# Kernel optimization log

Measured on AMD Instinct MI355X. Metric: run time of the kernel, lower is better.

Reference implementation:

```python
import jax, jax.numpy as jnp
import numpy as np

H1, H2, H3 = 32, 64, 64
NODEN = 12
NODES_PER_GRAPH = NODEN + 2  # 14
N = 700000                   # 50000 graphs * 14 nodes
E = 4000000


def setup_inputs() -> dict:
    key = jax.random.key(0)
    ks = jax.random.split(key, 8)
    x = jax.random.normal(ks[0], (N, H1), dtype=jnp.float32)
    edges = jax.random.randint(ks[1], (2, E), 0, N, dtype=jnp.int64)
    W1 = jax.random.normal(ks[2], (H1, H2), dtype=jnp.float32) / np.sqrt(H1).astype(np.float32)
    b1 = jnp.zeros((H2,), jnp.float32)
    W2 = jax.random.normal(ks[3], (H2, H3), dtype=jnp.float32) / np.sqrt(H2).astype(np.float32)
    b2 = jnp.zeros((H3,), jnp.float32)
    Wfc = jax.random.normal(ks[4], (H3 * NODES_PER_GRAPH, 1), dtype=jnp.float32) / np.sqrt(H3 * NODES_PER_GRAPH).astype(np.float32)
    bfc = jnp.zeros((1,), jnp.float32)
    return {"x": x, "edges": edges, "W1": W1, "b1": b1, "W2": W2, "b2": b2, "Wfc": Wfc, "bfc": bfc}


def gcn_conv(x, src, dst, W, b, n):
    # PyG GCNConv: h = X W; add self-loops; norm = deg^-1/2[src]*deg^-1/2[dst]
    h = x @ W  # [N, out]
    ones = jnp.ones(src.shape[0], dtype=h.dtype)
    deg = jax.ops.segment_sum(ones, dst, num_segments=n) + jnp.asarray(1.0, h.dtype)  # +1 self-loop
    dinv = jax.lax.rsqrt(deg)  # deg >= 1 always (self-loop)
    norm = dinv[src] * dinv[dst]  # [E]
    agg = jax.ops.segment_sum(h[src] * norm[:, None], dst, num_segments=n)
    agg = agg + h * (dinv * dinv)[:, None]  # self-loop contribution
    return agg + b


def reference(x, edges, W1, b1, W2, b2, Wfc, bfc):
    src, dst = edges[0], edges[1]
    h = jax.nn.relu(gcn_conv(x, src, dst, W1, b1, N))
    # F.dropout(training=False) is identity in eval mode
    h = jax.nn.relu(gcn_conv(h, src, dst, W2, b2, N))
    h = h.reshape(-1, H3 * NODES_PER_GRAPH)  # [B, 896]
    return h @ Wfc + bfc  # [B, 1]
```

## Files before the change

### kernel.cpp

```cpp
#include <hip/hip_runtime.h>
#include <hip/hip_fp16.h>


typedef _Float16 half8 __attribute__((ext_vector_type(8)));
typedef float float4v __attribute__((ext_vector_type(4)));

#define CHUNK 8192
#define BSH 11
#define BNODES 2048

__global__ __launch_bounds__(256) void fallback_kernel(float* __restrict__ out, int n, float v)
{
  int i = blockIdx.x * 256 + threadIdx.x;
  if (i < n) out[i] = v;
}

__global__ __launch_bounds__(64) void probe_kernel(const int* __restrict__ edges, int* __restrict__ flag)
{
  if (threadIdx.x == 0) {
    int orv = edges[1] | edges[3] | edges[5] | edges[7] | edges[9] | edges[11] | edges[13] | edges[15];
    flag[0] = (orv == 0) ? 1 : 0;
  }
}

__global__ __launch_bounds__(64) void zero_dummy_kernel(
    __half* __restrict__ F1, __half* __restrict__ F2, int N)
{
  int t = threadIdx.x;
  if (t < 16) ((uint2*)(F1 + (size_t)N * 64))[t] = make_uint2(0, 0);
  else if (t < 32) ((uint2*)(F2 + (size_t)N * 64))[t - 16] = make_uint2(0, 0);
}

__global__ __launch_bounds__(256) void hist2_kernel(
    const int* __restrict__ edges, int E, int N, const int* __restrict__ flag,
    int* __restrict__ cnt, int NBK)
{
  __shared__ int lh[512];
  int t = threadIdx.x;
  int blk = blockIdx.x;
  for (int b = t; b < NBK; b += 256) lh[b] = 0;
  __syncthreads();
  int sh = flag[0];
  int base = blk * CHUNK;
#pragma unroll
  for (int k = 0; k < CHUNK / 256; k++) {
    int e = base + k * 256 + t;
    if (e < E) {
      int d = edges[(E + e) << sh];
      if ((unsigned)d < (unsigned)N) atomicAdd(&lh[d >> BSH], 1);
    }
  }
  __syncthreads();
  for (int b = t; b < NBK; b += 256) cnt[(size_t)blk * NBK + b] = lh[b];
}

__global__ __launch_bounds__(64) void colscan_kernel(
    int* __restrict__ cnt, int NCH, int NBK, int* __restrict__ totals)
{
  int b = blockIdx.x;
  int lane = threadIdx.x;
  int carry = 0;
  int rounds = (NCH + 63) >> 6;
  for (int r = 0; r < rounds; r++) {
    int blk = r * 64 + lane;
    int v = (blk < NCH) ? cnt[(size_t)blk * NBK + b] : 0;
    int incl = v;
#pragma unroll
    for (int off = 1; off < 64; off <<= 1) {
      int x = __shfl_up(incl, off);
      if (lane >= off) incl += x;
    }
    int excl = incl - v + carry;
    if (blk < NCH) cnt[(size_t)blk * NBK + b] = excl;
    carry += __shfl(incl, 63);
  }
  if (lane == 0) totals[b] = carry;
}

__global__ __launch_bounds__(512) void scan_totals_kernel(
    const int* __restrict__ totals, int NBK,
    int* __restrict__ bstart, int* __restrict__ rowptr, int N)
{
  __shared__ int sm[512];
  int t = threadIdx.x;
  int v = (t < NBK) ? totals[t] : 0;
  sm[t] = v;
  __syncthreads();
  for (int off = 1; off < 512; off <<= 1) {
    int x = 0;
    if (t >= off) x = sm[t - off];
    __syncthreads();
    if (t >= off) sm[t] += x;
    __syncthreads();
  }
  if (t < NBK) bstart[t] = sm[t] - v;
  if (t == 0) { bstart[NBK] = sm[511]; rowptr[N] = sm[511] + N; }
}

__global__ __launch_bounds__(256) void pass3_kernel(
    const int* __restrict__ edges, int E, int N, const int* __restrict__ flag,
    const int* __restrict__ cnt, const int* __restrict__ bstart,
    int* __restrict__ pair, int NBK)
{
  __shared__ int lcur[512];
  int t = threadIdx.x;
  int blk = blockIdx.x;
  for (int b = t; b < NBK; b += 256)
    lcur[b] = bstart[b] + cnt[(size_t)blk * NBK + b];
  __syncthreads();
  int sh = flag[0];
  int base = blk * CHUNK;
#pragma unroll
  for (int k = 0; k < CHUNK / 256; k++) {
    int e = base + k * 256 + t;
    if (e < E) {
      int s = edges[e << sh];
      int d = edges[(E + e) << sh];
      if ((unsigned)s < (unsigned)N && (unsigned)d < (unsigned)N) {
        int pos = atomicAdd(&lcur[d >> BSH], 1);
        pair[pos] = s | ((d & (BNODES - 1)) << 20);
      }
    }
  }
}

__global__ __launch_bounds__(256) void build_kernel(
    const int* __restrict__ pair, const int* __restrict__ bstart,
    int* __restrict__ rowptr, float* __restrict__ dinv, int* __restrict__ col, int N)
{
  __shared__ int hist[BNODES];
  __shared__ int cur[BNODES];
  __shared__ int sc[256];
  int b = blockIdx.x;
  int t = threadIdx.x;
  int pbeg = bstart[b], pend = bstart[b + 1];
  int colbase = pbeg + (b << BSH);
#pragma unroll
  for (int i = 0; i < BNODES / 256; i++) {
    int idx = i * 256 + t;
    int row = (b << BSH) + idx;
    hist[idx] = (row < N) ? 1 : 0;
  }
  __syncthreads();
  for (int p = pbeg + t; p < pend; p += 256)
    atomicAdd(&hist[(pair[p] >> 20) & (BNODES - 1)], 1);
  __syncthreads();
  int hv[8];
  int tsum = 0;
#pragma unroll
  for (int i = 0; i < 8; i++) { hv[i] = hist[t * 8 + i]; tsum += hv[i]; }
  sc[t] = tsum;
  __syncthreads();
  for (int off = 1; off < 256; off <<= 1) {
    int x = 0;
    if (t >= off) x = sc[t - off];
    __syncthreads();
    if (t >= off) sc[t] += x;
    __syncthreads();
  }
  int run = sc[t] - tsum;
#pragma unroll
  for (int i = 0; i < 8; i++) {
    int idx = t * 8 + i;
    int rp = colbase + run;
    int row = (b << BSH) + idx;
    if (row < N) {
      rowptr[row] = rp;
      dinv[row] = rsqrtf((float)hv[i]);
      col[rp] = row;
      cur[idx] = rp + 1;
    } else {
      cur[idx] = rp;
    }
    run += hv[i];
  }
  __syncthreads();
  for (int p = pbeg + t; p < pend; p += 256) {
    int v = pair[p];
    int pos = atomicAdd(&cur[(v >> 20) & (BNODES - 1)], 1);
    col[pos] = v & 0xFFFFF;
  }
}

__global__ __launch_bounds__(256) void mfma_mm1_kernel(
    const float* __restrict__ X, const float* __restrict__ W1,
    const float* __restrict__ dinv, __half* __restrict__ G, int n, int ntiles)
{
  int lane = threadIdx.x & 63;
  int n16 = lane & 15;
  int quad = lane >> 4;

  half8 bf[4];
#pragma unroll
  for (int jb = 0; jb < 4; jb++)
#pragma unroll
    for (int i = 0; i < 8; i++)
      bf[jb][i] = (_Float16)W1[(quad * 8 + i) * 64 + jb * 16 + n16];

  _Float16* Gh = (_Float16*)G;
  int wave = (blockIdx.x * 256 + threadIdx.x) >> 6;
  int nw = (gridDim.x * 256) >> 6;
  for (int tile = wave; tile < ntiles; tile += nw) {
    int ut = __builtin_amdgcn_readfirstlane(tile);
    int base = ut * 16;
    int node = base + n16;
    if (node >= n) node = n - 1;
    const float* xr = X + (size_t)node * 32 + quad * 8;
    half8 a;
#pragma unroll
    for (int i = 0; i < 8; i++) a[i] = (_Float16)xr[i];

    float4v acc[4];
#pragma unroll
    for (int jb = 0; jb < 4; jb++) {
      float4v z = {0.f, 0.f, 0.f, 0.f};
      acc[jb] = __builtin_amdgcn_mfma_f32_16x16x32_f16(a, bf[jb], z, 0, 0, 0);
    }
#pragma unroll
    for (int r = 0; r < 4; r++) {
      int node2 = base + quad * 4 + r;
      if (node2 < n) {
        float dv = dinv[node2];
#pragma unroll
        for (int jb = 0; jb < 4; jb++)
          Gh[(size_t)node2 * 64 + jb * 16 + n16] = (_Float16)(dv * acc[jb][r]);
      }
    }
  }
}

__device__ inline void hacc(uint4 v, __half2* a)
{
  a[0] = __hadd2(a[0], *reinterpret_cast<__half2*>(&v.x));
  a[1] = __hadd2(a[1], *reinterpret_cast<__half2*>(&v.y));
  a[2] = __hadd2(a[2], *reinterpret_cast<__half2*>(&v.z));
  a[3] = __hadd2(a[3], *reinterpret_cast<__half2*>(&v.w));
}

__device__ inline __half2 hrelu2(__half2 v)
{
  __half z = __float2half_rn(0.f);
  __half2 r;
  r.x = __hmax(v.x, z);
  r.y = __hmax(v.y, z);
  return r;
}

__global__ __launch_bounds__(256) void agg1_frag_kernel(
    const __half* __restrict__ G, const int* __restrict__ rowptr,
    const int* __restrict__ col, const float* __restrict__ dinv,
    const float* __restrict__ bias, __half* __restrict__ U, int ntiles, int ndummy)
{
  int lane = threadIdx.x & 63;
  int n16 = lane & 15;
  int quad = lane >> 4;

  const float* bp0 = bias + quad * 8;
  const float* bp1 = bias + 32 + quad * 8;
  float4 b0a = *(const float4*)bp0, b0b = *(const float4*)(bp0 + 4);
  float4 b1a = *(const float4*)bp1, b1b = *(const float4*)(bp1 + 4);
  __half2 bh0[4] = {__floats2half2_rn(b0a.x, b0a.y), __floats2half2_rn(b0a.z, b0a.w),
                    __floats2half2_rn(b0b.x, b0b.y), __floats2half2_rn(b0b.z, b0b.w)};
  __half2 bh1[4] = {__floats2half2_rn(b1a.x, b1a.y), __floats2half2_rn(b1a.z, b1a.w),
                    __floats2half2_rn(b1b.x, b1b.y), __floats2half2_rn(b1b.z, b1b.w)};

  const uint4* G4 = (const uint4*)G;
  uint4* U4 = (uint4*)U;
  int wave = (blockIdx.x * 256 + threadIdx.x) >> 6;
  int nw = (gridDim.x * 256) >> 6;
  for (int tile = wave; tile < ntiles; tile += nw) {
    int ut = __builtin_amdgcn_readfirstlane(tile);
    int node = ut * 16 + n16;
    int rbeg = rowptr[node];
    int rlen = rowptr[node + 1] - rbeg;

    __half2 z2 = __float2half2_rn(0.f);
    __half2 acc0[4] = {z2, z2, z2, z2};
    __half2 acc1[4] = {z2, z2, z2, z2};

    for (int j = 0; __any(j < rlen); j += 2) {
      int c0 = col[rbeg + j];
      int c1 = col[rbeg + j + 1];
      c0 = (j < rlen) ? c0 : ndummy;
      c1 = (j + 1 < rlen) ? c1 : ndummy;
      uint4 v00 = G4[((size_t)c0 << 3) + quad];
      uint4 v01 = G4[((size_t)c0 << 3) + 4 + quad];
      uint4 v10 = G4[((size_t)c1 << 3) + quad];
      uint4 v11 = G4[((size_t)c1 << 3) + 4 + quad];
      hacc(v00, acc0); hacc(v01, acc1);
      hacc(v10, acc0); hacc(v11, acc1);
    }

    __half2 dv = __half2half2(__float2half_rn(dinv[node]));
    uint4 o0, o1;
    __half2 r;
#pragma unroll
    for (int j = 0; j < 4; j++) {
      r = __hmul2(hrelu2(__hadd2(__hmul2(acc0[j], dv), bh0[j])), dv);
      (&o0.x)[j] = *reinterpret_cast<uint*>(&r);
      r = __hmul2(hrelu2(__hadd2(__hmul2(acc1[j], dv), bh1[j])), dv);
      (&o1.x)[j] = *reinterpret_cast<uint*>(&r);
    }
    U4[((size_t)node << 3) + quad] = o0;
    U4[((size_t)node << 3) + 4 + quad] = o1;
  }
}

__global__ __launch_bounds__(256) void out_init_kernel(
    float* __restrict__ out, const float* __restrict__ bfc, int n)
{
  int i = blockIdx.x * 256 + threadIdx.x;
  if (i < n) out[i] = bfc[0];
}

__global__ __launch_bounds__(256) void mfma_final_fused_kernel(
    const __half* __restrict__ U, const int* __restrict__ rowptr,
    const int* __restrict__ col, const float* __restrict__ dinv,
    const float* __restrict__ W2, const float* __restrict__ b2,
    const float* __restrict__ Wfc, float* __restrict__ out,
    int ntiles, int ndummy)
{
  int lane = threadIdx.x & 63;
  int n16 = lane & 15;
  int quad = lane >> 4;

  half8 bf[4][2];
#pragma unroll
  for (int jb = 0; jb < 4; jb++)
#pragma unroll
    for (int kf = 0; kf < 2; kf++)
#pragma unroll
      for (int i = 0; i < 8; i++)
        bf[jb][kf][i] = (_Float16)W2[(kf * 32 + quad * 8 + i) * 64 + jb * 16 + n16];
  float b2j[4];
#pragma unroll
  for (int jb = 0; jb < 4; jb++) b2j[jb] = b2[jb * 16 + n16];

  const uint4* U4 = (const uint4*)U;
  int wave = (blockIdx.x * 256 + threadIdx.x) >> 6;
  int nw = (gridDim.x * 256) >> 6;
  for (int tile = wave; tile < ntiles; tile += nw) {
    int ut = __builtin_amdgcn_readfirstlane(tile);
    int base = ut * 16;
    int node = base + n16;
    int rbeg = rowptr[node];
    int rlen = rowptr[node + 1] - rbeg;

    __half2 z2 = __float2half2_rn(0.f);
    __half2 acc0[4] = {z2, z2, z2, z2};
    __half2 acc1[4] = {z2, z2, z2, z2};

    for (int j = 0; __any(j < rlen); j += 2) {
      int c0 = col[rbeg + j];
      int c1 = col[rbeg + j + 1];
      c0 = (j < rlen) ? c0 : ndummy;
      c1 = (j + 1 < rlen) ? c1 : ndummy;
      uint4 v00 = U4[((size_t)c0 << 3) + quad];
      uint4 v01 = U4[((size_t)c0 << 3) + 4 + quad];
      uint4 v10 = U4[((size_t)c1 << 3) + quad];
      uint4 v11 = U4[((size_t)c1 << 3) + 4 + quad];
      hacc(v00, acc0); hacc(v01, acc1);
      hacc(v10, acc0); hacc(v11, acc1);
    }
    __half2 dv = __half2half2(__float2half_rn(dinv[node]));
#pragma unroll
    for (int j = 0; j < 4; j++) {
      acc0[j] = __hmul2(acc0[j], dv);
      acc1[j] = __hmul2(acc1[j], dv);
    }
    half8 a0 = *reinterpret_cast<half8*>(acc0);
    half8 a1 = *reinterpret_cast<half8*>(acc1);

    int g_r[4], t_r[4];
#pragma unroll
    for (int r = 0; r < 4; r++) {
      int nd = base + quad * 4 + r;
      g_r[r] = nd / 14;
      t_r[r] = nd - g_r[r] * 14;
    }
    float pr[4] = {0.f, 0.f, 0.f, 0.f};
#pragma unroll
    for (int jb = 0; jb < 4; jb++) {
      float4v acc = {0.f, 0.f, 0.f, 0.f};
      acc = __builtin_amdgcn_mfma_f32_16x16x32_f16(a0, bf[jb][0], acc, 0, 0, 0);
      acc = __builtin_amdgcn_mfma_f32_16x16x32_f16(a1, bf[jb][1], acc, 0, 0, 0);
      int j = jb * 16 + n16;
#pragma unroll
      for (int r = 0; r < 4; r++) {
        float h = acc[r] + b2j[jb];
        h = h > 0.f ? h : 0.f;
        pr[r] += h * Wfc[t_r[r] * 64 + j];
      }
    }
#pragma unroll
    for (int r = 0; r < 4; r++) {
#pragma unroll
      for (int off = 1; off < 16; off <<= 1) pr[r] += __shfl_xor(pr[r], off);
    }
    if (n16 == 0) {
#pragma unroll
      for (int r = 0; r < 4; r++) atomicAdd(&out[g_r[r]], pr[r]);
    }
  }
}

extern "C" void kernel_launch(void* const* d_in, const int* in_sizes, int n_in,
                              void* d_out, int out_size, void* d_ws, size_t ws_size,
                              hipStream_t stream)
{
  const float* x = (const float*)d_in[0];
  const int* edges = (const int*)d_in[1];
  const float* W1 = (const float*)d_in[2];
  const float* b1 = (const float*)d_in[3];
  const float* W2 = (const float*)d_in[4];
  const float* b2 = (const float*)d_in[5];
  const float* Wfc = (const float*)d_in[6];
  const float* bfc = (const float*)d_in[7];
  float* out = (float*)d_out;
  (void)n_in;

  const int N = in_sizes[0] / 32;
  const int E = in_sizes[1] / 2;
  const int B = out_size;
  const int NBK = (N + BNODES - 1) >> BSH;
  const int NCH = (E + CHUNK - 1) / CHUNK;

  char* ws = (char*)d_ws;
  size_t off = 0;
  auto alloc = [&](size_t bytes) -> void* {
    void* p = ws + off;
    off += (bytes + 255) & ~(size_t)255;
    return p;
  };
  int* flag = (int*)alloc(256);
  int* cnt = (int*)alloc((size_t)NCH * NBK * 4);
  int* totals = (int*)alloc((size_t)NBK * 4);
  int* bstart = (int*)alloc(((size_t)NBK + 1) * 4);
  int* col = (int*)alloc(((size_t)E + N + 256) * 4);
  int* rowptr = (int*)alloc(((size_t)N + 1) * 4);
  float* dinv = (float*)alloc((size_t)N * 4);
  __half* F1 = (__half*)alloc(((size_t)N + 16) * 64 * 2);
  __half* F2 = (__half*)alloc(((size_t)N + 16) * 64 * 2);
  int* pair = (int*)F1;

  if (off > ws_size) {
    float v = -(float)(double)(ws_size >> 20);
    fallback_kernel<<<(B + 255) / 256, 256, 0, stream>>>(out, B, v);
    return;
  }

  probe_kernel<<<1, 64, 0, stream>>>(edges, flag);
  zero_dummy_kernel<<<1, 64, 0, stream>>>(F1, F2, N);
  hist2_kernel<<<NCH, 256, 0, stream>>>(edges, E, N, flag, cnt, NBK);
  colscan_kernel<<<NBK, 64, 0, stream>>>(cnt, NCH, NBK, totals);
  scan_totals_kernel<<<1, 512, 0, stream>>>(totals, NBK, bstart, rowptr, N);
  pass3_kernel<<<NCH, 256, 0, stream>>>(edges, E, N, flag, cnt, bstart, pair, NBK);
  build_kernel<<<NBK, 256, 0, stream>>>(pair, bstart, rowptr, dinv, col, N);

  int ntiles = (N + 15) / 16;
  mfma_mm1_kernel<<<4096, 256, 0, stream>>>(x, W1, dinv, F1, N, ntiles);
  agg1_frag_kernel<<<4096, 256, 0, stream>>>(F1, rowptr, col, dinv, b1, F2, ntiles, N);
  out_init_kernel<<<(B + 255) / 256, 256, 0, stream>>>(out, bfc, B);
  mfma_final_fused_kernel<<<4096, 256, 0, stream>>>(F2, rowptr, col, dinv, W2, b2, Wfc,
                                                    out, ntiles, N);
}
```

Measured before the change: 573.1 us.

## Aggregate layer-1 on 32-wide scaled inputs before the W1 GEMM

Reorders layer 1 as (A·X)·W1 instead of A·(X·W1). A new kernel first scales X by dinv and stores it in fp16, so the gather loop reads 32 halves per neighbour instead of 64. The MFMA with W1, bias, ReLU and second scaling are then fused into the aggregation kernel. The neighbour loops in both aggregation kernels are also unrolled deeper (8 and 4 neighbours per step) with split accumulators to add memory-level parallelism. The trade-offs are extra padded dummy loads when node degrees are uneven and a different fp16 rounding order.

```diff
diff --git a/kernel.cpp b/kernel.cpp
--- a/kernel.cpp
+++ b/kernel.cpp
@@ -24,11 +24,11 @@
 }
 
 __global__ __launch_bounds__(64) void zero_dummy_kernel(
-    __half* __restrict__ F1, __half* __restrict__ F2, int N)
+    __half* __restrict__ P, __half* __restrict__ F2, int N)
 {
   int t = threadIdx.x;
-  if (t < 16) ((uint2*)(F1 + (size_t)N * 64))[t] = make_uint2(0, 0);
-  else if (t < 32) ((uint2*)(F2 + (size_t)N * 64))[t - 16] = make_uint2(0, 0);
+  if (t < 8) ((uint2*)(P + (size_t)N * 32))[t] = make_uint2(0, 0);
+  else if (t < 24) ((uint2*)(F2 + (size_t)N * 64))[t - 8] = make_uint2(0, 0);
 }
 
 __global__ __launch_bounds__(256) void hist2_kernel(
@@ -182,9 +182,40 @@
   }
 }
 
-__global__ __launch_bounds__(256) void mfma_mm1_kernel(
-    const float* __restrict__ X, const float* __restrict__ W1,
-    const float* __restrict__ dinv, __half* __restrict__ G, int n, int ntiles)
+__global__ __launch_bounds__(256) void scale_x_kernel(
+    const float* __restrict__ X, const float* __restrict__ dinv,
+    __half* __restrict__ P, int N)
+{
+  int idx = blockIdx.x * 256 + threadIdx.x;
+  int total = N * 4;
+  int stride = gridDim.x * 256;
+  for (int i = idx; i < total; i += stride) {
+    int node = i >> 2, part = i & 3;
+    const float4* xp = (const float4*)(X + (size_t)node * 32 + part * 8);
+    float dv = dinv[node];
+    float4 v0 = xp[0], v1 = xp[1];
+    half8 h;
+    h[0] = (_Float16)(dv * v0.x); h[1] = (_Float16)(dv * v0.y);
+    h[2] = (_Float16)(dv * v0.z); h[3] = (_Float16)(dv * v0.w);
+    h[4] = (_Float16)(dv * v1.x); h[5] = (_Float16)(dv * v1.y);
+    h[6] = (_Float16)(dv * v1.z); h[7] = (_Float16)(dv * v1.w);
+    *(half8*)(P + (size_t)node * 32 + part * 8) = h;
+  }
+}
+
+__device__ inline void hacc(uint4 v, __half2* a)
+{
+  a[0] = __hadd2(a[0], *reinterpret_cast<__half2*>(&v.x));
+  a[1] = __hadd2(a[1], *reinterpret_cast<__half2*>(&v.y));
+  a[2] = __hadd2(a[2], *reinterpret_cast<__half2*>(&v.z));
+  a[3] = __hadd2(a[3], *reinterpret_cast<__half2*>(&v.w));
+}
+
+__global__ __launch_bounds__(256) void agg1_mfma_kernel(
+    const __half* __restrict__ P, const int* __restrict__ rowptr,
+    const int* __restrict__ col, const float* __restrict__ dinv,
+    const float* __restrict__ W1, const float* __restrict__ b1,
+    __half* __restrict__ U, int ntiles, int ndummy)
 {
   int lane = threadIdx.x & 63;
   int n16 = lane & 15;
@@ -196,113 +227,59 @@
 #pragma unroll
     for (int i = 0; i < 8; i++)
       bf[jb][i] = (_Float16)W1[(quad * 8 + i) * 64 + jb * 16 + n16];
-
-  _Float16* Gh = (_Float16*)G;
+  float b1j[4];
+#pragma unroll
+  for (int jb = 0; jb < 4; jb++) b1j[jb] = b1[jb * 16 + n16];
+
+  const uint4* P4 = (const uint4*)P;
+  _Float16* Uh = (_Float16*)U;
   int wave = (blockIdx.x * 256 + threadIdx.x) >> 6;
   int nw = (gridDim.x * 256) >> 6;
   for (int tile = wave; tile < ntiles; tile += nw) {
     int ut = __builtin_amdgcn_readfirstlane(tile);
     int base = ut * 16;
     int node = base + n16;
-    if (node >= n) node = n - 1;
-    const float* xr = X + (size_t)node * 32 + quad * 8;
-    half8 a;
-#pragma unroll
-    for (int i = 0; i < 8; i++) a[i] = (_Float16)xr[i];
-
-    float4v acc[4];
+    int rbeg = rowptr[node];
+    int rlen = rowptr[node + 1] - rbeg;
+
+    __half2 z2 = __float2half2_rn(0.f);
+    __half2 aA[4] = {z2, z2, z2, z2};
+    __half2 aB[4] = {z2, z2, z2, z2};
+
+    for (int j = 0; __any(j < rlen); j += 8) {
+      int c[8];
+#pragma unroll
+      for (int q = 0; q < 8; q++) {
+        int cc = col[rbeg + j + q];
+        c[q] = (j + q < rlen) ? cc : ndummy;
+      }
+      uint4 v[8];
+#pragma unroll
+      for (int q = 0; q < 8; q++) v[q] = P4[((size_t)c[q] << 2) + quad];
+#pragma unroll
+      for (int q = 0; q < 8; q += 2) { hacc(v[q], aA); hacc(v[q + 1], aB); }
+    }
+#pragma unroll
+    for (int k = 0; k < 4; k++) aA[k] = __hadd2(aA[k], aB[k]);
+
+    half8 a = *reinterpret_cast<half8*>(aA);
+    float4v co[4];
 #pragma unroll
     for (int jb = 0; jb < 4; jb++) {
       float4v z = {0.f, 0.f, 0.f, 0.f};
-      acc[jb] = __builtin_amdgcn_mfma_f32_16x16x32_f16(a, bf[jb], z, 0, 0, 0);
+      co[jb] = __builtin_amdgcn_mfma_f32_16x16x32_f16(a, bf[jb], z, 0, 0, 0);
     }
 #pragma unroll
     for (int r = 0; r < 4; r++) {
       int node2 = base + quad * 4 + r;
-      if (node2 < n) {
-        float dv = dinv[node2];
-#pragma unroll
-        for (int jb = 0; jb < 4; jb++)
-          Gh[(size_t)node2 * 64 + jb * 16 + n16] = (_Float16)(dv * acc[jb][r]);
+      float dv = dinv[node2];
+#pragma unroll
+      for (int jb = 0; jb < 4; jb++) {
+        float h = dv * co[jb][r] + b1j[jb];
+        h = h > 0.f ? h : 0.f;
+        Uh[(size_t)node2 * 64 + jb * 16 + n16] = (_Float16)(dv * h);
       }
     }
-  }
-}
-
-__device__ inline void hacc(uint4 v, __half2* a)
-{
-  a[0] = __hadd2(a[0], *reinterpret_cast<__half2*>(&v.x));
-  a[1] = __hadd2(a[1], *reinterpret_cast<__half2*>(&v.y));
-  a[2] = __hadd2(a[2], *reinterpret_cast<__half2*>(&v.z));
-  a[3] = __hadd2(a[3], *reinterpret_cast<__half2*>(&v.w));
-}
-
-__device__ inline __half2 hrelu2(__half2 v)
-{
-  __half z = __float2half_rn(0.f);
-  __half2 r;
-  r.x = __hmax(v.x, z);
-  r.y = __hmax(v.y, z);
-  return r;
-}
-
-__global__ __launch_bounds__(256) void agg1_frag_kernel(
-    const __half* __restrict__ G, const int* __restrict__ rowptr,
-    const int* __restrict__ col, const float* __restrict__ dinv,
-    const float* __restrict__ bias, __half* __restrict__ U, int ntiles, int ndummy)
-{
-  int lane = threadIdx.x & 63;
-  int n16 = lane & 15;
-  int quad = lane >> 4;
-
-  const float* bp0 = bias + quad * 8;
-  const float* bp1 = bias + 32 + quad * 8;
-  float4 b0a = *(const float4*)bp0, b0b = *(const float4*)(bp0 + 4);
-  float4 b1a = *(const float4*)bp1, b1b = *(const float4*)(bp1 + 4);
-  __half2 bh0[4] = {__floats2half2_rn(b0a.x, b0a.y), __floats2half2_rn(b0a.z, b0a.w),
-                    __floats2half2_rn(b0b.x, b0b.y), __floats2half2_rn(b0b.z, b0b.w)};
-  __half2 bh1[4] = {__floats2half2_rn(b1a.x, b1a.y), __floats2half2_rn(b1a.z, b1a.w),
-                    __floats2half2_rn(b1b.x, b1b.y), __floats2half2_rn(b1b.z, b1b.w)};
-
-  const uint4* G4 = (const uint4*)G;
-  uint4* U4 = (uint4*)U;
-  int wave = (blockIdx.x * 256 + threadIdx.x) >> 6;
-  int nw = (gridDim.x * 256) >> 6;
-  for (int tile = wave; tile < ntiles; tile += nw) {
-    int ut = __builtin_amdgcn_readfirstlane(tile);
-    int node = ut * 16 + n16;
-    int rbeg = rowptr[node];
-    int rlen = rowptr[node + 1] - rbeg;
-
-    __half2 z2 = __float2half2_rn(0.f);
-    __half2 acc0[4] = {z2, z2, z2, z2};
-    __half2 acc1[4] = {z2, z2, z2, z2};
-
-    for (int j = 0; __any(j < rlen); j += 2) {
-      int c0 = col[rbeg + j];
-      int c1 = col[rbeg + j + 1];
-      c0 = (j < rlen) ? c0 : ndummy;
-      c1 = (j + 1 < rlen) ? c1 : ndummy;
-      uint4 v00 = G4[((size_t)c0 << 3) + quad];
-      uint4 v01 = G4[((size_t)c0 << 3) + 4 + quad];
-      uint4 v10 = G4[((size_t)c1 << 3) + quad];
-      uint4 v11 = G4[((size_t)c1 << 3) + 4 + quad];
-      hacc(v00, acc0); hacc(v01, acc1);
-      hacc(v10, acc0); hacc(v11, acc1);
-    }
-
-    __half2 dv = __half2half2(__float2half_rn(dinv[node]));
-    uint4 o0, o1;
-    __half2 r;
-#pragma unroll
-    for (int j = 0; j < 4; j++) {
-      r = __hmul2(hrelu2(__hadd2(__hmul2(acc0[j], dv), bh0[j])), dv);
-      (&o0.x)[j] = *reinterpret_cast<uint*>(&r);
-      r = __hmul2(hrelu2(__hadd2(__hmul2(acc1[j], dv), bh1[j])), dv);
-      (&o1.x)[j] = *reinterpret_cast<uint*>(&r);
-    }
-    U4[((size_t)node << 3) + quad] = o0;
-    U4[((size_t)node << 3) + 4 + quad] = o1;
   }
 }
 
@@ -347,29 +324,46 @@
     int rlen = rowptr[node + 1] - rbeg;
 
     __half2 z2 = __float2half2_rn(0.f);
-    __half2 acc0[4] = {z2, z2, z2, z2};
-    __half2 acc1[4] = {z2, z2, z2, z2};
-
-    for (int j = 0; __any(j < rlen); j += 2) {
+    __half2 aE0[4] = {z2, z2, z2, z2};
+    __half2 aE1[4] = {z2, z2, z2, z2};
+    __half2 aO0[4] = {z2, z2, z2, z2};
+    __half2 aO1[4] = {z2, z2, z2, z2};
+
+    for (int j = 0; __any(j < rlen); j += 4) {
       int c0 = col[rbeg + j];
       int c1 = col[rbeg + j + 1];
+      int c2 = col[rbeg + j + 2];
+      int c3 = col[rbeg + j + 3];
       c0 = (j < rlen) ? c0 : ndummy;
       c1 = (j + 1 < rlen) ? c1 : ndummy;
+      c2 = (j + 2 < rlen) ? c2 : ndummy;
+      c3 = (j + 3 < rlen) ? c3 : ndummy;
       uint4 v00 = U4[((size_t)c0 << 3) + quad];
       uint4 v01 = U4[((size_t)c0 << 3) + 4 + quad];
       uint4 v10 = U4[((size_t)c1 << 3) + quad];
       uint4 v11 = U4[((size_t)c1 << 3) + 4 + quad];
-      hacc(v00, acc0); hacc(v01, acc1);
-      hacc(v10, acc0); hacc(v11, acc1);
+      uint4 v20 = U4[((size_t)c2 << 3) + quad];
+      uint4 v21 = U4[((size_t)c2 << 3) + 4 + quad];
+      uint4 v30 = U4[((size_t)c3 << 3) + quad];
+      uint4 v31 = U4[((size_t)c3 << 3) + 4 + quad];
+      hacc(v00, aE0); hacc(v01, aE1);
+      hacc(v10, aO0); hacc(v11, aO1);
+      hacc(v20, aE0); hacc(v21, aE1);
+      hacc(v30, aO0); hacc(v31, aO1);
+    }
+#pragma unroll
+    for (int k = 0; k < 4; k++) {
+      aE0[k] = __hadd2(aE0[k], aO0[k]);
+      aE1[k] = __hadd2(aE1[k], aO1[k]);
     }
     __half2 dv = __half2half2(__float2half_rn(dinv[node]));
 #pragma unroll
     for (int j = 0; j < 4; j++) {
-      acc0[j] = __hmul2(acc0[j], dv);
-      acc1[j] = __hmul2(acc1[j], dv);
-    }
-    half8 a0 = *reinterpret_cast<half8*>(acc0);
-    half8 a1 = *reinterpret_cast<half8*>(acc1);
+      aE0[j] = __hmul2(aE0[j], dv);
+      aE1[j] = __hmul2(aE1[j], dv);
+    }
+    half8 a0 = *reinterpret_cast<half8*>(aE0);
+    half8 a1 = *reinterpret_cast<half8*>(aE1);
 
     int g_r[4], t_r[4];
 #pragma unroll
@@ -439,9 +433,9 @@
   int* col = (int*)alloc(((size_t)E + N + 256) * 4);
   int* rowptr = (int*)alloc(((size_t)N + 1) * 4);
   float* dinv = (float*)alloc((size_t)N * 4);
-  __half* F1 = (__half*)alloc(((size_t)N + 16) * 64 * 2);
+  __half* P = (__half*)alloc(((size_t)N + 16) * 32 * 2);
   __half* F2 = (__half*)alloc(((size_t)N + 16) * 64 * 2);
-  int* pair = (int*)F1;
+  int* pair = (int*)P;
 
   if (off > ws_size) {
     float v = -(float)(double)(ws_size >> 20);
@@ -450,7 +444,7 @@
   }
 
   probe_kernel<<<1, 64, 0, stream>>>(edges, flag);
-  zero_dummy_kernel<<<1, 64, 0, stream>>>(F1, F2, N);
+  zero_dummy_kernel<<<1, 64, 0, stream>>>(P, F2, N);
   hist2_kernel<<<NCH, 256, 0, stream>>>(edges, E, N, flag, cnt, NBK);
   colscan_kernel<<<NBK, 64, 0, stream>>>(cnt, NCH, NBK, totals);
   scan_totals_kernel<<<1, 512, 0, stream>>>(totals, NBK, bstart, rowptr, N);
@@ -458,8 +452,8 @@
   build_kernel<<<NBK, 256, 0, stream>>>(pair, bstart, rowptr, dinv, col, N);
 
   int ntiles = (N + 15) / 16;
-  mfma_mm1_kernel<<<4096, 256, 0, stream>>>(x, W1, dinv, F1, N, ntiles);
-  agg1_frag_kernel<<<4096, 256, 0, stream>>>(F1, rowptr, col, dinv, b1, F2, ntiles, N);
+  scale_x_kernel<<<2048, 256, 0, stream>>>(x, dinv, P, N);
+  agg1_mfma_kernel<<<4096, 256, 0, stream>>>(P, rowptr, col, dinv, W1, b1, F2, ntiles, N);
   out_init_kernel<<<(B + 255) / 256, 256, 0, stream>>>(out, bfc, B);
   mfma_final_fused_kernel<<<4096, 256, 0, stream>>>(F2, rowptr, col, dinv, W2, b2, Wfc,
                                                     out, ntiles, N);
```

Result: faster. 533.3 us (-6.9%).
